# Optimization experiments

Hardware: AMD Instinct MI355X
Metric: run time of the kernel (lower is better)

The kernel has to match this reference:

```python
import jax, jax.numpy as jnp
import numpy as np

SEQ_LEN = 8192
D_K = 128
NEG_BIG = 1000000000.0


def setup_inputs() -> dict:
    key = jax.random.key(0)
    kq, kk, kv = jax.random.split(key, 3)
    q = jax.random.normal(kq, (SEQ_LEN, D_K), dtype=jnp.float32)
    k = jax.random.normal(kk, (SEQ_LEN, D_K), dtype=jnp.float32)
    v = jax.random.normal(kv, (SEQ_LEN, D_K), dtype=jnp.float32)
    return {"q": q, "k": k, "v": v}


def reference(q, k, v):
    # q,k,v: (S, d). Naive attention with causal (look-ahead) mask, masked=True.
    d_k = q.shape[-1]
    scaled_logits = jnp.matmul(q, k.T) / jnp.sqrt(jnp.asarray(d_k, q.dtype))  # (S, S)
    look_ahead_mask = jnp.triu(jnp.ones((SEQ_LEN, SEQ_LEN), dtype=q.dtype), k=1)
    scaled_logits = scaled_logits - look_ahead_mask * NEG_BIG
    attn = jnp.matmul(jax.nn.softmax(scaled_logits, axis=-1), v)  # (S, d)
    return attn
```

## Files before the change

### kernel.cpp

```cpp
#include <hip/hip_runtime.h>
#include <hip/hip_bf16.h>
#include <math.h>

#define S_LEN 8192
#define DK    128
#define BM    128
#define BN    64
#define NQT   (S_LEN / BM)
#define NW    8
#define SCALE 0.08838834764831845f

typedef __bf16 bf16x8_t __attribute__((ext_vector_type(8)));
typedef __bf16 bf16x4_t __attribute__((ext_vector_type(4)));
typedef __bf16 bf16x2_t __attribute__((ext_vector_type(2)));
typedef float  floatx4  __attribute__((ext_vector_type(4)));

#define GLD16(g, l) __builtin_amdgcn_global_load_lds(                      \
    (const __attribute__((address_space(1))) void*)(g),                    \
    (__attribute__((address_space(3))) void*)(l), 16, 0, 0)

__global__ __launch_bounds__(256)
void prep(const float* __restrict__ Q, const float* __restrict__ K,
          const float* __restrict__ V, __bf16* __restrict__ Qb,
          __bf16* __restrict__ Kb, __bf16* __restrict__ Vt) {
  const int b = blockIdx.x;
  __shared__ __bf16 t[64][DK + 8];
  if (b < 2048) {
    const float* src = (b < 1024) ? Q : K;
    __bf16* dst = (b < 1024) ? Qb : Kb;
    const int i = ((b & 1023) * 256 + threadIdx.x) * 4;
    float4 v = *(const float4*)&src[i];
    bf16x4_t o;
    o[0] = (__bf16)v.x; o[1] = (__bf16)v.y; o[2] = (__bf16)v.z; o[3] = (__bf16)v.w;
    *(bf16x4_t*)&dst[i] = o;
  } else {
    const int tid  = threadIdx.x;
    const int key0 = (b - 2048) * 64;
    {
      const int r = tid >> 2, cg = (tid & 3) * 32;
      const float* vp = V + (size_t)(key0 + r) * DK + cg;
      #pragma unroll
      for (int i = 0; i < 8; ++i) {
        float4 v = ((const float4*)vp)[i];
        bf16x4_t o;
        o[0]=(__bf16)v.x; o[1]=(__bf16)v.y; o[2]=(__bf16)v.z; o[3]=(__bf16)v.w;
        *(bf16x4_t*)&t[r][cg + i * 4] = o;
      }
    }
    __syncthreads();
    const int d = tid >> 1, h = (tid & 1) * 32;
    __bf16* op = Vt + (size_t)d * S_LEN + key0 + h;
    #pragma unroll
    for (int jb = 0; jb < 4; ++jb) {
      bf16x8_t o;
      #pragma unroll
      for (int j = 0; j < 8; ++j) o[j] = t[h + jb * 8 + j][d];
      *(bf16x8_t*)&op[jb * 8] = o;
    }
  }
}

__global__ __launch_bounds__(512, 4)
void fa_part(const __bf16* __restrict__ Qb, const __bf16* __restrict__ Kb,
             const __bf16* __restrict__ Vtg, __bf16* __restrict__ Opart,
             float* __restrict__ Odirect, float* __restrict__ stats,
             int G, int direct) {
  __shared__ __align__(16) __bf16 Ks[BN * DK];
  __shared__ __align__(16) __bf16 Vts[DK * BN];
  __shared__ __align__(16) __bf16 Pl[NW][16][BN + 8];

  const int tid  = threadIdx.x;
  const int wave = tid >> 6;
  const int lane = tid & 63;
  const int l15  = lane & 15;
  const int quad = lane >> 4;

  const int qtile = blockIdx.x;
  const int g     = blockIdx.y;
  const int nt    = 2 * qtile + 2;
  const int Ci    = (nt + G - 1) / G;
  const int jb0   = g * Ci;
  const int jb1   = (jb0 + Ci < nt) ? (jb0 + Ci) : nt;
  const int chunk = qtile * G + g;

  if (jb0 >= jb1) {
    if (tid < BM) {
      stats[((size_t)chunk * BM + tid) * 2 + 0] = -INFINITY;
      stats[((size_t)chunk * BM + tid) * 2 + 1] = 0.f;
    }
    return;
  }

  const int q0w = qtile * BM + wave * 16;

  bf16x8_t qf[4];
  #pragma unroll
  for (int kb = 0; kb < 4; ++kb)
    qf[kb] = *(const bf16x8_t*)&Qb[(size_t)(q0w + l15) * DK + kb * 32 + quad * 8];

  const __bf16* kp[2]; const __bf16* vp[2];
  const __bf16* kl[2]; const __bf16* vl[2];
  #pragma unroll
  for (int t = 0; t < 2; ++t) {
    const int s  = wave * 2 + t;
    const int rk = 4 * s + (lane >> 4);
    const int ck = (lane & 15) ^ (rk & 15);
    kp[t] = Kb + ((size_t)jb0 * BN + rk) * DK + ck * 8;
    kl[t] = Ks + s * 512;
    const int rv = 8 * s + (lane >> 3);
    const int cv = (lane & 7) ^ (rv & 7);
    vp[t] = Vtg + (size_t)rv * S_LEN + jb0 * BN + cv * 8;
    vl[t] = Vts + s * 512;
  }

  floatx4 o_acc[8];
  #pragma unroll
  for (int dt = 0; dt < 8; ++dt) o_acc[dt] = (floatx4){0.f, 0.f, 0.f, 0.f};
  float m_r[4], l_r[4];
  #pragma unroll
  for (int r = 0; r < 4; ++r) { m_r[r] = -INFINITY; l_r[r] = 0.f; }

  for (int jb = jb0; jb < jb1; ++jb) {
    const int key0 = jb * BN;

    #pragma unroll
    for (int t = 0; t < 2; ++t) {
      GLD16(kp[t], kl[t]);
      GLD16(vp[t], vl[t]);
      kp[t] += BN * DK;
      vp[t] += BN;
    }
    __syncthreads();

    if (key0 <= q0w + 15) {
      floatx4 sv[4];
      #pragma unroll
      for (int n = 0; n < 4; ++n) {
        floatx4 acc = (floatx4){0.f, 0.f, 0.f, 0.f};
        #pragma unroll
        for (int kb = 0; kb < 4; ++kb) {
          bf16x8_t bfr = *(const bf16x8_t*)
              &Ks[(n * 16 + l15) * DK + (((kb * 4 + quad) ^ l15) * 8)];
          acc = __builtin_amdgcn_mfma_f32_16x16x32_bf16(qf[kb], bfr, acc, 0, 0, 0);
        }
        sv[n] = acc;
      }

      if (key0 + BN - 1 > q0w) {
        #pragma unroll
        for (int n = 0; n < 4; ++n) {
          const int key = key0 + n * 16 + l15;
          #pragma unroll
          for (int r = 0; r < 4; ++r) {
            const int qi = q0w + quad * 4 + r;
            float v = sv[n][r] * SCALE;
            sv[n][r] = (key > qi) ? -1e30f : v;
          }
        }
      } else {
        #pragma unroll
        for (int n = 0; n < 4; ++n)
          #pragma unroll
          for (int r = 0; r < 4; ++r) sv[n][r] *= SCALE;
      }

      float rm[4];
      #pragma unroll
      for (int r = 0; r < 4; ++r)
        rm[r] = fmaxf(fmaxf(sv[0][r], sv[1][r]), fmaxf(sv[2][r], sv[3][r]));
      #pragma unroll
      for (int off = 8; off >= 1; off >>= 1) {
        #pragma unroll
        for (int r = 0; r < 4; ++r) rm[r] = fmaxf(rm[r], __shfl_xor(rm[r], off));
      }
      float alpha[4];
      #pragma unroll
      for (int r = 0; r < 4; ++r) {
        const float mn = fmaxf(m_r[r], rm[r]);
        alpha[r] = __expf(m_r[r] - mn);
        m_r[r] = mn;
      }
      float rs[4] = {0.f, 0.f, 0.f, 0.f};
      #pragma unroll
      for (int n = 0; n < 4; ++n) {
        #pragma unroll
        for (int r = 0; r < 4; ++r) {
          const float p = __expf(sv[n][r] - m_r[r]);
          sv[n][r] = p;
          rs[r] += p;
        }
      }
      #pragma unroll
      for (int off = 8; off >= 1; off >>= 1) {
        #pragma unroll
        for (int r = 0; r < 4; ++r) rs[r] += __shfl_xor(rs[r], off);
      }
      #pragma unroll
      for (int r = 0; r < 4; ++r) l_r[r] = l_r[r] * alpha[r] + rs[r];
      #pragma unroll
      for (int dt = 0; dt < 8; ++dt)
        #pragma unroll
        for (int r = 0; r < 4; ++r) o_acc[dt][r] *= alpha[r];

      #pragma unroll
      for (int n = 0; n < 4; ++n)
        #pragma unroll
        for (int r = 0; r < 4; ++r)
          Pl[wave][quad * 4 + r][n * 16 + l15] = (__bf16)sv[n][r];

      #pragma unroll
      for (int kc = 0; kc < 2; ++kc) {
        bf16x8_t af = *(const bf16x8_t*)&Pl[wave][l15][kc * 32 + quad * 8];
        #pragma unroll
        for (int dt = 0; dt < 8; ++dt) {
          bf16x8_t vf = *(const bf16x8_t*)
              &Vts[(dt * 16 + l15) * BN + (((kc * 4 + quad) ^ (l15 & 7)) * 8)];
          o_acc[dt] = __builtin_amdgcn_mfma_f32_16x16x32_bf16(af, vf, o_acc[dt], 0, 0, 0);
        }
      }
    }
    __syncthreads();
  }

  if (direct) {
    #pragma unroll
    for (int r = 0; r < 4; ++r) {
      const float inv = 1.0f / l_r[r];
      float* orow = Odirect + (size_t)(q0w + quad * 4 + r) * DK + l15;
      #pragma unroll
      for (int dt = 0; dt < 8; ++dt) orow[dt * 16] = o_acc[dt][r] * inv;
    }
  } else {
    #pragma unroll
    for (int r = 0; r < 4; ++r) {
      const int row = wave * 16 + quad * 4 + r;
      __bf16* orow = Opart + ((size_t)chunk * BM + row) * DK + l15;
      #pragma unroll
      for (int dt = 0; dt < 8; ++dt) orow[dt * 16] = (__bf16)o_acc[dt][r];
    }
    if (l15 == 0) {
      #pragma unroll
      for (int r = 0; r < 4; ++r) {
        const int row = wave * 16 + quad * 4 + r;
        stats[((size_t)chunk * BM + row) * 2 + 0] = m_r[r];
        stats[((size_t)chunk * BM + row) * 2 + 1] = l_r[r];
      }
    }
  }
}

template <int GF>
__device__ __forceinline__ void reduce_body(const __bf16* __restrict__ Opart,
                                            const float* __restrict__ stats,
                                            float* __restrict__ O, int G) {
  const int wave = threadIdx.x >> 6, lane = threadIdx.x & 63;
  const int row = blockIdx.x * 4 + wave;
  const int qt = row >> 7, r = row & 127;
  const int n = (GF > 0) ? GF : G;

  float M = -INFINITY;
  #pragma unroll
  for (int g = 0; g < n; ++g)
    M = fmaxf(M, stats[((size_t)(qt * n + g) * BM + r) * 2]);

  float L = 0.f, ax = 0.f, ay = 0.f;
  #pragma unroll
  for (int g = 0; g < n; ++g) {
    const size_t sidx = (size_t)(qt * n + g) * BM + r;
    const float m = stats[sidx * 2];
    const float w = (m == -INFINITY) ? 0.f : __expf(m - M);
    L += stats[sidx * 2 + 1] * w;
    bf16x2_t o = *(const bf16x2_t*)&Opart[sidx * DK + lane * 2];
    ax += w * (float)o[0];
    ay += w * (float)o[1];
  }
  const float inv = 1.f / L;
  float2 res; res.x = ax * inv; res.y = ay * inv;
  *(float2*)&O[(size_t)row * DK + lane * 2] = res;
}

__global__ __launch_bounds__(256)
void fa_reduce(const __bf16* __restrict__ Opart, const float* __restrict__ stats,
               float* __restrict__ O, int G) {
  if (G == 8) reduce_body<8>(Opart, stats, O, G);
  else        reduce_body<0>(Opart, stats, O, G);
}

extern "C" void kernel_launch(void* const* d_in, const int* in_sizes, int n_in,
                              void* d_out, int out_size, void* d_ws, size_t ws_size,
                              hipStream_t stream) {
  (void)in_sizes; (void)n_in; (void)out_size;
  const float* q = (const float*)d_in[0];
  const float* k = (const float*)d_in[1];
  const float* v = (const float*)d_in[2];
  float* out = (float*)d_out;

  const size_t conv = 3 * (size_t)S_LEN * DK * 2;
  const size_t per_g = (size_t)NQT * BM * DK * 2
                     + (size_t)NQT * BM * 2 * sizeof(float);
  int G = 1;
  if (ws_size > conv + 2 * per_g) {
    G = (int)((ws_size - conv) / per_g);
    if (G > 8) G = 8;
  }

  __bf16* Qb = (__bf16*)d_ws;
  __bf16* Kb = Qb + (size_t)S_LEN * DK;
  __bf16* Vt = Kb + (size_t)S_LEN * DK;
  __bf16* Opart = Vt + (size_t)S_LEN * DK;
  float* stats = (float*)(Opart + (size_t)NQT * G * BM * DK);

  prep<<<2176, 256, 0, stream>>>(q, k, v, Qb, Kb, Vt);

  if (G >= 2) {
    fa_part<<<dim3(NQT, G), 512, 0, stream>>>(Qb, Kb, Vt, Opart, nullptr, stats, G, 0);
    fa_reduce<<<S_LEN / 4, 256, 0, stream>>>(Opart, stats, out, G);
  } else {
    fa_part<<<dim3(NQT, 1), 512, 0, stream>>>(Qb, Kb, Vt, Opart, out, stats, 1, 1);
  }
}
```

Measured before the change: 141.6 us.

## Prefetch K/V tiles via registers, fold scale into K, drop Q conversion, raise split count

```diff
diff --git a/kernel.cpp b/kernel.cpp
--- a/kernel.cpp
+++ b/kernel.cpp
@@ -8,6 +8,7 @@
 #define BN    64
 #define NQT   (S_LEN / BM)
 #define NW    8
+#define GMAX  16
 #define SCALE 0.08838834764831845f
 
 typedef __bf16 bf16x8_t __attribute__((ext_vector_type(8)));
@@ -15,32 +16,26 @@
 typedef __bf16 bf16x2_t __attribute__((ext_vector_type(2)));
 typedef float  floatx4  __attribute__((ext_vector_type(4)));
 
-#define GLD16(g, l) __builtin_amdgcn_global_load_lds(                      \
-    (const __attribute__((address_space(1))) void*)(g),                    \
-    (__attribute__((address_space(3))) void*)(l), 16, 0, 0)
-
 __global__ __launch_bounds__(256)
-void prep(const float* __restrict__ Q, const float* __restrict__ K,
-          const float* __restrict__ V, __bf16* __restrict__ Qb,
+void prep(const float* __restrict__ K, const float* __restrict__ V,
           __bf16* __restrict__ Kb, __bf16* __restrict__ Vt) {
+  __shared__ __bf16 t[32][DK + 8];
   const int b = blockIdx.x;
-  __shared__ __bf16 t[64][DK + 8];
-  if (b < 2048) {
-    const float* src = (b < 1024) ? Q : K;
-    __bf16* dst = (b < 1024) ? Qb : Kb;
-    const int i = ((b & 1023) * 256 + threadIdx.x) * 4;
-    float4 v = *(const float4*)&src[i];
+  if (b < 1024) {
+    const int i = (b * 256 + threadIdx.x) * 4;
+    float4 v = *(const float4*)&K[i];
     bf16x4_t o;
-    o[0] = (__bf16)v.x; o[1] = (__bf16)v.y; o[2] = (__bf16)v.z; o[3] = (__bf16)v.w;
-    *(bf16x4_t*)&dst[i] = o;
+    o[0] = (__bf16)(v.x * SCALE); o[1] = (__bf16)(v.y * SCALE);
+    o[2] = (__bf16)(v.z * SCALE); o[3] = (__bf16)(v.w * SCALE);
+    *(bf16x4_t*)&Kb[i] = o;
   } else {
     const int tid  = threadIdx.x;
-    const int key0 = (b - 2048) * 64;
+    const int key0 = (b - 1024) * 32;
     {
-      const int r = tid >> 2, cg = (tid & 3) * 32;
+      const int r = tid >> 3, cg = (tid & 7) * 16;
       const float* vp = V + (size_t)(key0 + r) * DK + cg;
       #pragma unroll
-      for (int i = 0; i < 8; ++i) {
+      for (int i = 0; i < 4; ++i) {
         float4 v = ((const float4*)vp)[i];
         bf16x4_t o;
         o[0]=(__bf16)v.x; o[1]=(__bf16)v.y; o[2]=(__bf16)v.z; o[3]=(__bf16)v.w;
@@ -48,10 +43,10 @@
       }
     }
     __syncthreads();
-    const int d = tid >> 1, h = (tid & 1) * 32;
+    const int d = tid >> 1, h = (tid & 1) * 16;
     __bf16* op = Vt + (size_t)d * S_LEN + key0 + h;
     #pragma unroll
-    for (int jb = 0; jb < 4; ++jb) {
+    for (int jb = 0; jb < 2; ++jb) {
       bf16x8_t o;
       #pragma unroll
       for (int j = 0; j < 8; ++j) o[j] = t[h + jb * 8 + j][d];
@@ -61,7 +56,7 @@
 }
 
 __global__ __launch_bounds__(512, 4)
-void fa_part(const __bf16* __restrict__ Qb, const __bf16* __restrict__ Kb,
+void fa_part(const float* __restrict__ Q, const __bf16* __restrict__ Kb,
              const __bf16* __restrict__ Vtg, __bf16* __restrict__ Opart,
              float* __restrict__ Odirect, float* __restrict__ stats,
              int G, int direct) {
@@ -94,23 +89,41 @@
   const int q0w = qtile * BM + wave * 16;
 
   bf16x8_t qf[4];
-  #pragma unroll
-  for (int kb = 0; kb < 4; ++kb)
-    qf[kb] = *(const bf16x8_t*)&Qb[(size_t)(q0w + l15) * DK + kb * 32 + quad * 8];
+  {
+    const float* qrow = Q + (size_t)(q0w + l15) * DK + quad * 8;
+    #pragma unroll
+    for (int kb = 0; kb < 4; ++kb) {
+      const float4* p = (const float4*)(qrow + kb * 32);
+      float4 a = p[0], b = p[1];
+      bf16x8_t f;
+      f[0]=(__bf16)a.x; f[1]=(__bf16)a.y; f[2]=(__bf16)a.z; f[3]=(__bf16)a.w;
+      f[4]=(__bf16)b.x; f[5]=(__bf16)b.y; f[6]=(__bf16)b.z; f[7]=(__bf16)b.w;
+      qf[kb] = f;
+    }
+  }
 
   const __bf16* kp[2]; const __bf16* vp[2];
-  const __bf16* kl[2]; const __bf16* vl[2];
+  __bf16* kl[2]; __bf16* vl[2];
   #pragma unroll
   for (int t = 0; t < 2; ++t) {
     const int s  = wave * 2 + t;
     const int rk = 4 * s + (lane >> 4);
     const int ck = (lane & 15) ^ (rk & 15);
     kp[t] = Kb + ((size_t)jb0 * BN + rk) * DK + ck * 8;
-    kl[t] = Ks + s * 512;
+    kl[t] = Ks + s * 512 + lane * 8;
     const int rv = 8 * s + (lane >> 3);
     const int cv = (lane & 7) ^ (rv & 7);
     vp[t] = Vtg + (size_t)rv * S_LEN + jb0 * BN + cv * 8;
-    vl[t] = Vts + s * 512;
+    vl[t] = Vts + s * 512 + lane * 8;
+  }
+
+  bf16x8_t kr[2], vr[2];
+  #pragma unroll
+  for (int t = 0; t < 2; ++t) {
+    kr[t] = *(const bf16x8_t*)kp[t];
+    vr[t] = *(const bf16x8_t*)vp[t];
+    kp[t] += BN * DK;
+    vp[t] += BN;
   }
 
   floatx4 o_acc[8];
@@ -121,17 +134,25 @@
   for (int r = 0; r < 4; ++r) { m_r[r] = -INFINITY; l_r[r] = 0.f; }
 
   for (int jb = jb0; jb < jb1; ++jb) {
+    __syncthreads();
+    #pragma unroll
+    for (int t = 0; t < 2; ++t) {
+      *(bf16x8_t*)kl[t] = kr[t];
+      *(bf16x8_t*)vl[t] = vr[t];
+    }
+    __syncthreads();
+
+    if (jb + 1 < jb1) {
+      #pragma unroll
+      for (int t = 0; t < 2; ++t) {
+        kr[t] = *(const bf16x8_t*)kp[t];
+        vr[t] = *(const bf16x8_t*)vp[t];
+        kp[t] += BN * DK;
+        vp[t] += BN;
+      }
+    }
+
     const int key0 = jb * BN;
-
-    #pragma unroll
-    for (int t = 0; t < 2; ++t) {
-      GLD16(kp[t], kl[t]);
-      GLD16(vp[t], vl[t]);
-      kp[t] += BN * DK;
-      vp[t] += BN;
-    }
-    __syncthreads();
-
     if (key0 <= q0w + 15) {
       floatx4 sv[4];
       #pragma unroll
@@ -153,15 +174,9 @@
           #pragma unroll
           for (int r = 0; r < 4; ++r) {
             const int qi = q0w + quad * 4 + r;
-            float v = sv[n][r] * SCALE;
-            sv[n][r] = (key > qi) ? -1e30f : v;
+            sv[n][r] = (key > qi) ? -1e30f : sv[n][r];
           }
         }
-      } else {
-        #pragma unroll
-        for (int n = 0; n < 4; ++n)
-          #pragma unroll
-          for (int r = 0; r < 4; ++r) sv[n][r] *= SCALE;
       }
 
       float rm[4];
@@ -219,7 +234,6 @@
         }
       }
     }
-    __syncthreads();
   }
 
   if (direct) {
@@ -282,8 +296,9 @@
 __global__ __launch_bounds__(256)
 void fa_reduce(const __bf16* __restrict__ Opart, const float* __restrict__ stats,
                float* __restrict__ O, int G) {
-  if (G == 8) reduce_body<8>(Opart, stats, O, G);
-  else        reduce_body<0>(Opart, stats, O, G);
+  if      (G == 16) reduce_body<16>(Opart, stats, O, G);
+  else if (G == 8)  reduce_body<8>(Opart, stats, O, G);
+  else              reduce_body<0>(Opart, stats, O, G);
 }
 
 extern "C" void kernel_launch(void* const* d_in, const int* in_sizes, int n_in,
@@ -295,27 +310,26 @@
   const float* v = (const float*)d_in[2];
   float* out = (float*)d_out;
 
-  const size_t conv = 3 * (size_t)S_LEN * DK * 2;
+  const size_t conv = 2 * (size_t)S_LEN * DK * 2;
   const size_t per_g = (size_t)NQT * BM * DK * 2
                      + (size_t)NQT * BM * 2 * sizeof(float);
   int G = 1;
   if (ws_size > conv + 2 * per_g) {
     G = (int)((ws_size - conv) / per_g);
-    if (G > 8) G = 8;
-  }
-
-  __bf16* Qb = (__bf16*)d_ws;
-  __bf16* Kb = Qb + (size_t)S_LEN * DK;
+    if (G > GMAX) G = GMAX;
+  }
+
+  __bf16* Kb = (__bf16*)d_ws;
   __bf16* Vt = Kb + (size_t)S_LEN * DK;
   __bf16* Opart = Vt + (size_t)S_LEN * DK;
   float* stats = (float*)(Opart + (size_t)NQT * G * BM * DK);
 
-  prep<<<2176, 256, 0, stream>>>(q, k, v, Qb, Kb, Vt);
+  prep<<<1280, 256, 0, stream>>>(k, v, Kb, Vt);
 
   if (G >= 2) {
-    fa_part<<<dim3(NQT, G), 512, 0, stream>>>(Qb, Kb, Vt, Opart, nullptr, stats, G, 0);
+    fa_part<<<dim3(NQT, G), 512, 0, stream>>>(q, Kb, Vt, Opart, nullptr, stats, G, 0);
     fa_reduce<<<S_LEN / 4, 256, 0, stream>>>(Opart, stats, out, G);
   } else {
-    fa_part<<<dim3(NQT, 1), 512, 0, stream>>>(Qb, Kb, Vt, Opart, out, stats, 1, 1);
-  }
-}
+    fa_part<<<dim3(NQT, 1), 512, 0, stream>>>(q, Kb, Vt, Opart, out, stats, 1, 1);
+  }
+}
```

Result: slower. 151.1 us (+6.7%).
